# Kernel optimization log

Measured on AMD Instinct MI355X. Metric: run time of the kernel, lower is better.

Reference implementation:

```python
import jax, jax.numpy as jnp
import numpy as np

B, T, C = 1, 2048, 2048
H, KV, D = 16, 4, 128
PAST = 2048


def setup_inputs() -> dict:
    key = jax.random.key(0)
    ks = jax.random.split(key, 11)
    return {
        "x": jax.random.normal(ks[0], (B, T, C), jnp.float32),
        "ve": jax.random.normal(ks[1], (B, T, KV * D), jnp.float32),
        "cos": jax.random.normal(ks[2], (1, T, 1, D // 2), jnp.float32),
        "sin": jax.random.normal(ks[3], (1, T, 1, D // 2), jnp.float32),
        "past_key": jax.random.normal(ks[4], (B, PAST, KV, D), jnp.float32),
        "past_value": jax.random.normal(ks[5], (B, PAST, KV, D), jnp.float32),
        "Wq": jax.random.normal(ks[6], (C, H * D), jnp.float32) * 0.02,
        "Wk": jax.random.normal(ks[7], (C, KV * D), jnp.float32) * 0.02,
        "Wv": jax.random.normal(ks[8], (C, KV * D), jnp.float32) * 0.02,
        "Wo": jax.random.normal(ks[9], (H * D, C), jnp.float32) * 0.02,
        "Wg": jax.random.normal(ks[10], (12, KV), jnp.float32),
    }


def _rmsnorm(x):
    return x * jax.lax.rsqrt(jnp.mean(x * x, axis=-1, keepdims=True) + 1e-6)


def _rope(x, cos, sin):
    # x: (B,T,heads,D); cos/sin: (1,T,1,D//2) broadcast over heads
    d = x.shape[-1] // 2
    x1, x2 = x[..., :d], x[..., d:]
    return jnp.concatenate([x1 * cos + x2 * sin, -x1 * sin + x2 * cos], axis=-1)


def reference(x, ve, cos, sin, past_key, past_value, Wq, Wk, Wv, Wo, Wg):
    Bx, Tx, Cx = x.shape
    G = H // KV
    q = (x @ Wq).reshape(Bx, Tx, H, D)
    k = (x @ Wk).reshape(Bx, Tx, KV, D)
    v = (x @ Wv).reshape(Bx, Tx, KV, D)
    # value-embedding gate: 3*sigmoid over first 12 channels of x
    gate = 3.0 * jax.nn.sigmoid(x[..., :12] @ Wg)  # (B,T,KV)
    v = v + gate[..., None] * ve.reshape(Bx, Tx, KV, D)
    q = _rmsnorm(_rope(q, cos, sin)) * 1.2
    k = _rmsnorm(_rope(k, cos, sin)) * 1.2
    present_key = jnp.concatenate([past_key, k], axis=1)    # (B,S,KV,D)
    present_value = jnp.concatenate([past_value, v], axis=1)
    S = present_key.shape[1]
    q_t = q.transpose(0, 2, 1, 3)                           # (B,H,T,D)
    k_t = present_key.transpose(0, 2, 1, 3)                 # (B,KV,S,D)
    v_t = present_value.transpose(0, 2, 1, 3)
    # GQA expansion: repeat each kv head G times -> (B,H,S,D)
    k_t = jnp.broadcast_to(k_t[:, :, None], (Bx, KV, G, S, D)).reshape(Bx, H, S, D)
    v_t = jnp.broadcast_to(v_t[:, :, None], (Bx, KV, G, S, D)).reshape(Bx, H, S, D)
    scale = D ** -0.5
    scores = jnp.einsum("bhtd,bhsd->bhts", q_t, k_t) * scale
    query_pos = jnp.arange(S - Tx, S)[:, None]
    key_pos = jnp.arange(S)[None, :]
    causal = key_pos <= query_pos                           # (T,S)
    scores = jnp.where(causal[None, None], scores, -jnp.inf)
    w = jax.nn.softmax(scores, axis=-1)
    y = jnp.einsum("bhts,bhsd->bthd", w, v_t).reshape(Bx, Tx, H * D)
    y = y @ Wo
    return (y, present_key, present_value)
```

## Files before the change

kernel.cpp:

```cpp
#include <hip/hip_runtime.h>
#include <hip/hip_bf16.h>
#include <math.h>

typedef __attribute__((ext_vector_type(8))) short short8;
typedef __attribute__((ext_vector_type(4))) short short4v;
typedef __attribute__((ext_vector_type(4))) float f32x4;

#define DEV __device__ __forceinline__

DEV short f2bf(float f) {
  unsigned u = __builtin_bit_cast(unsigned, f);
  unsigned r = (u + 0x7FFFu + ((u >> 16) & 1u)) >> 16;
  return (short)r;
}

DEV short f2h(float f) {
  _Float16 h = (_Float16)f;
  return __builtin_bit_cast(short, h);
}

DEV float h2f(short s) {
  return (float)__builtin_bit_cast(_Float16, s);
}

DEV unsigned cvt_pk_bf16(float lo, float hi) {
  unsigned r;
  asm("v_cvt_pk_bf16_f32 %0, %1, %2" : "=v"(r) : "v"(lo), "v"(hi));
  return r;
}

DEV void gload_lds16(const void* g, void* l) {
  __builtin_amdgcn_global_load_lds((const __attribute__((address_space(1))) void*)g,
                                   (__attribute__((address_space(3))) void*)l, 16, 0, 0);
}

__global__ __launch_bounds__(256) void gemm_bf16(const short* __restrict__ A,
                                                 const short* __restrict__ BT,
                                                 float* __restrict__ C,
                                                 int M, int N, int K) {
  __shared__ __attribute__((aligned(16))) short As[2][128 * 32];
  __shared__ __attribute__((aligned(16))) short Bs[2][128 * 32];
  const int tid = threadIdx.x;
  const int w = tid >> 6, l = tid & 63;
  const int g = l >> 4, lr = l & 15;
  int nbx = gridDim.x, nwg = nbx * gridDim.y;
  int flat = blockIdx.y * nbx + blockIdx.x;
  int qq = nwg >> 3;
  int f2 = (flat & 7) * qq + (flat >> 3);
  const int m0 = (f2 / nbx) * 128, n0 = (f2 % nbx) * 128;
  const int wr = w >> 1, wc = w & 1;
  const int q0 = w * 2, q1 = w * 2 + 1;
  const int e0 = q0 * 512 + l * 8, e1 = q1 * 512 + l * 8;
  const int ra = e0 >> 5, ka = e0 & 31;
  const int rb_ = e1 >> 5, kb_ = e1 & 31;
  f32x4 acc[4][4] = {};

  auto stage = [&](int buf, int k0) {
    gload_lds16(A + (size_t)(m0 + ra) * K + k0 + ka, As[buf] + q0 * 512);
    gload_lds16(BT + (size_t)(n0 + ra) * K + k0 + ka, Bs[buf] + q0 * 512);
    gload_lds16(A + (size_t)(m0 + rb_) * K + k0 + kb_, As[buf] + q1 * 512);
    gload_lds16(BT + (size_t)(n0 + rb_) * K + k0 + kb_, Bs[buf] + q1 * 512);
  };

  stage(0, 0);
  __syncthreads();
  int cur = 0;
  for (int k0 = 0; k0 < K; k0 += 32) {
    if (k0 + 32 < K) stage(cur ^ 1, k0 + 32);
    short8 af[4], bfr[4];
#pragma unroll
    for (int i = 0; i < 4; ++i) {
      af[i] = *(const short8*)(As[cur] + (wr * 64 + i * 16 + lr) * 32 + g * 8);
      bfr[i] = *(const short8*)(Bs[cur] + (wc * 64 + i * 16 + lr) * 32 + g * 8);
    }
#pragma unroll
    for (int mi = 0; mi < 4; ++mi)
#pragma unroll
      for (int ni = 0; ni < 4; ++ni)
        acc[mi][ni] = __builtin_amdgcn_mfma_f32_16x16x32_bf16(af[mi], bfr[ni], acc[mi][ni], 0, 0, 0);
    __syncthreads();
    cur ^= 1;
  }
#pragma unroll
  for (int mi = 0; mi < 4; ++mi)
#pragma unroll
    for (int ni = 0; ni < 4; ++ni) {
      int row = m0 + wr * 64 + mi * 16 + g * 4;
      int col = n0 + wc * 64 + ni * 16 + lr;
#pragma unroll
      for (int r = 0; r < 4; ++r)
        C[(size_t)(row + r) * N + col] = acc[mi][ni][r];
    }
}

__global__ __launch_bounds__(256) void gemm_bf16_k64(const short* __restrict__ A,
                                                     const short* __restrict__ BT,
                                                     float* __restrict__ C,
                                                     int M, int N, int K) {
  __shared__ __attribute__((aligned(16))) short As[2][128 * 64];
  __shared__ __attribute__((aligned(16))) short Bs[2][128 * 64];
  const int tid = threadIdx.x;
  const int w = tid >> 6, l = tid & 63;
  const int g = l >> 4, lr = l & 15;
  int nbx = gridDim.x, nwg = nbx * gridDim.y;
  int flat = blockIdx.y * nbx + blockIdx.x;
  int qq = nwg >> 3;
  int f2 = (flat & 7) * qq + (flat >> 3);
  const int m0 = (f2 / nbx) * 128, n0 = (f2 % nbx) * 128;
  const int wr = w >> 1, wc = w & 1;
  f32x4 acc[4][4] = {};

  auto stage = [&](int buf, int k0) {
#pragma unroll
    for (int it = 0; it < 4; ++it) {
      int idx = it * 256 + tid;
      int row = idx >> 3;
      int colB = (idx & 7) * 16;
      int scol = colB ^ ((row & 7) << 4);
      gload_lds16(A + (size_t)(m0 + row) * K + k0 + (scol >> 1), As[buf] + idx * 8);
      gload_lds16(BT + (size_t)(n0 + row) * K + k0 + (scol >> 1), Bs[buf] + idx * 8);
    }
  };

  stage(0, 0);
  __syncthreads();
  int cur = 0;
  for (int k0 = 0; k0 < K; k0 += 64) {
    if (k0 + 64 < K) stage(cur ^ 1, k0 + 64);
#pragma unroll
    for (int ki = 0; ki < 2; ++ki) {
      short8 af[4], bfr[4];
#pragma unroll
      for (int i = 0; i < 4; ++i) {
        int off = ((wr * 64 + i * 16 + lr) * 128 + ((ki * 64 + g * 16) ^ ((lr & 7) << 4))) >> 1;
        int offb = ((wc * 64 + i * 16 + lr) * 128 + ((ki * 64 + g * 16) ^ ((lr & 7) << 4))) >> 1;
        af[i] = *(const short8*)(As[cur] + off);
        bfr[i] = *(const short8*)(Bs[cur] + offb);
      }
#pragma unroll
      for (int mi = 0; mi < 4; ++mi)
#pragma unroll
        for (int ni = 0; ni < 4; ++ni)
          acc[mi][ni] = __builtin_amdgcn_mfma_f32_16x16x32_bf16(af[mi], bfr[ni], acc[mi][ni], 0, 0, 0);
    }
    __syncthreads();
    cur ^= 1;
  }
#pragma unroll
  for (int mi = 0; mi < 4; ++mi)
#pragma unroll
    for (int ni = 0; ni < 4; ++ni) {
      int row = m0 + wr * 64 + mi * 16 + g * 4;
      int col = n0 + wc * 64 + ni * 16 + lr;
#pragma unroll
      for (int r = 0; r < 4; ++r)
        C[(size_t)(row + r) * N + col] = acc[mi][ni][r];
    }
}

__global__ __launch_bounds__(256) void transpose_all(const float* __restrict__ Wq,
                                                     const float* __restrict__ Wk,
                                                     const float* __restrict__ Wv,
                                                     const float* __restrict__ Wo,
                                                     short* __restrict__ WTqkv,
                                                     short* __restrict__ WToT) {
  __shared__ float tile[32][33];
  int bx = blockIdx.x;
  const float* W;
  short* WT;
  int N, cb;
  if (bx < 64) { W = Wq; WT = WTqkv; N = 2048; cb = bx; }
  else if (bx < 80) { W = Wk; WT = WTqkv + (size_t)2048 * 2048; N = 512; cb = bx - 64; }
  else if (bx < 96) { W = Wv; WT = WTqkv + (size_t)2560 * 2048; N = 512; cb = bx - 80; }
  else { W = Wo; WT = WToT; N = 2048; cb = bx - 96; }
  int tx = threadIdx.x, ty = threadIdx.y;
  int c0 = cb * 32, r0 = blockIdx.y * 32;
#pragma unroll
  for (int i = 0; i < 4; ++i)
    tile[ty + i * 8][tx] = W[(size_t)(r0 + ty + i * 8) * N + c0 + tx];
  __syncthreads();
#pragma unroll
  for (int i = 0; i < 4; ++i)
    WT[(size_t)(c0 + ty + i * 8) * 2048 + r0 + tx] = f2bf(tile[tx][ty + i * 8]);
}

__global__ __launch_bounds__(256) void cvt_x(const float* __restrict__ x,
                                             short* __restrict__ xb, int n4) {
  int i = blockIdx.x * 256 + threadIdx.x;
  if (i >= n4) return;
  float4 v = ((const float4*)x)[i];
  short4v o;
  o.x = f2bf(v.x); o.y = f2bf(v.y); o.z = f2bf(v.z); o.w = f2bf(v.w);
  ((short4v*)xb)[i] = o;
}

__global__ __launch_bounds__(256) void qkv_post(const float* __restrict__ qkv,
                                                const float* __restrict__ cosb,
                                                const float* __restrict__ sinb,
                                                const float* __restrict__ x,
                                                const float* __restrict__ ve,
                                                const float* __restrict__ Wg,
                                                float* __restrict__ outPK,
                                                float* __restrict__ outPV,
                                                short* __restrict__ qb,
                                                short* __restrict__ kb) {
  int gw = (blockIdx.x * 256 + threadIdx.x) >> 6;
  int l = threadIdx.x & 63;
  int t = gw / 24, u = gw - t * 24;
  if (t >= 2048) return;
  if (u < 20) {
    float c = cosb[t * 64 + l], s = sinb[t * 64 + l];
    const float* src = qkv + (size_t)t * 3072 + (u < 16 ? u * 128 : 2048 + (u - 16) * 128);
    float x1 = src[l], x2 = src[64 + l];
    float lo = x1 * c + x2 * s;
    float hi = x2 * c - x1 * s;
    float ss = lo * lo + hi * hi;
#pragma unroll
    for (int d = 1; d < 64; d <<= 1) ss += __shfl_xor(ss, d, 64);
    float r = rsqrtf(ss * (1.0f / 128.0f) + 1e-6f) * 1.2f;
    if (u < 16) {
      const float SCQ = 0.08838834764831845f * 1.4426950408889634f;
      float rq = r * SCQ;
      size_t b = ((size_t)u * 2048 + t) * 128;
      qb[b + l] = f2bf(lo * rq);
      qb[b + 64 + l] = f2bf(hi * rq);
    } else {
      lo *= r; hi *= r;
      int kvh = u - 16;
      size_t b = ((size_t)(2048 + t) * 4 + kvh) * 128;
      outPK[b + l] = lo;
      outPK[b + 64 + l] = hi;
      size_t b2 = ((size_t)kvh * 4096 + 2048 + t) * 128;
      kb[b2 + l] = f2bf(lo);
      kb[b2 + 64 + l] = f2bf(hi);
    }
  } else {
    int kv = u - 20;
    float z = 0.f;
#pragma unroll
    for (int j = 0; j < 12; ++j) z += x[(size_t)t * 2048 + j] * Wg[j * 4 + kv];
    float gate = 3.0f / (1.0f + expf(-z));
    const float* vr = qkv + (size_t)t * 3072 + 2560 + kv * 128;
    const float* vei = ve + (size_t)t * 512 + kv * 128;
    float v0 = vr[l] + gate * vei[l];
    float v1 = vr[64 + l] + gate * vei[64 + l];
    size_t b = ((size_t)(2048 + t) * 4 + kv) * 128;
    outPV[b + l] = v0;
    outPV[b + 64 + l] = v1;
  }
}

__global__ __launch_bounds__(256) void past_copy(const float* __restrict__ pk,
                                                 const float* __restrict__ pv,
                                                 float* __restrict__ outPK,
                                                 float* __restrict__ outPV,
                                                 short* __restrict__ kb) {
  int i = blockIdx.x * 256 + threadIdx.x;
  int d = i & 127, kv = (i >> 7) & 3, s = i >> 9;
  float a = pk[i], b = pv[i];
  outPK[i] = a;
  outPV[i] = b;
  kb[((size_t)kv * 4096 + s) * 128 + d] = f2bf(a);
}

__global__ __launch_bounds__(256) void v_transpose(const float* __restrict__ PV,
                                                   short* __restrict__ vbT) {
  __shared__ float tile[32][33];
  int tx = threadIdx.x, ty = threadIdx.y;
  int c0 = blockIdx.x * 32, r0 = blockIdx.y * 32;
#pragma unroll
  for (int i = 0; i < 4; ++i)
    tile[ty + i * 8][tx] = PV[(size_t)(r0 + ty + i * 8) * 512 + c0 + tx];
  __syncthreads();
#pragma unroll
  for (int i = 0; i < 4; ++i)
    vbT[(size_t)(c0 + ty + i * 8) * 4096 + r0 + tx] = f2bf(tile[tx][ty + i * 8]);
}

__global__ __launch_bounds__(256, 2) void attn(const short* __restrict__ qb,
                                               const short* __restrict__ kb,
                                               const short* __restrict__ vbT,
                                               short* __restrict__ Po,
                                               float* __restrict__ ml) {
  extern __shared__ __attribute__((aligned(16))) short smem[];
  short* Ks = smem;
  short* Vs = smem + 16384;
  const int tid = threadIdx.x, w = tid >> 6, l = tid & 63;
  const int g = l >> 4, lr = l & 15;
  const int lid = blockIdx.x;
  const int qbi = 15 - (lid >> 6);
  const int sub = lid & 63;
  const int h = sub >> 2, cls = sub & 3;
  const int kv = h >> 2;
  const int qw = qbi * 128 + w * 32;
  char* Pw = (char*)(smem + 32768) + w * 2048;
  const short* gK = kb + (size_t)kv * 4096 * 128;
  const short* gV = vbT + (size_t)kv * 128 * 4096;
  const int nT = 34 + 2 * qbi;
  const int cnt = (nT - cls + 3) >> 2;

  short8 aq[2][4];
#pragma unroll
  for (int u = 0; u < 2; ++u)
#pragma unroll
    for (int c4 = 0; c4 < 4; ++c4)
      aq[u][c4] = *(const short8*)(qb + ((size_t)(h * 2048 + qw + u * 16 + lr)) * 128 + c4 * 32 + g * 8);

  float m_r[2] = {-INFINITY, -INFINITY};
  float l_r[2] = {0.f, 0.f};
  f32x4 o[2][8] = {};

  auto stageK = [&](int buf, int s0) {
#pragma unroll
    for (int it = 0; it < 4; ++it) {
      int idx = it * 256 + tid;
      int row = idx >> 4;
      int colB = (idx & 15) * 16;
      int scol = colB ^ ((row & 7) << 4);
      gload_lds16(gK + (size_t)(s0 + row) * 128 + (scol >> 1),
                  Ks + buf * 8192 + (it * 256 + w * 64) * 8);
    }
  };
  auto stageV = [&](int buf, int s0) {
#pragma unroll
    for (int it = 0; it < 4; ++it) {
      int idx = it * 256 + tid;
      int row = idx >> 3;
      int colB = (idx & 7) * 16;
      int scol = colB ^ ((row & 7) << 4);
      gload_lds16(gV + (size_t)row * 4096 + s0 + (scol >> 1),
                  Vs + buf * 8192 + (it * 256 + w * 64) * 8);
    }
  };

  stageK(0, cls * 64);
  stageV(0, cls * 64);
  __syncthreads();
  int cur = 0;
  for (int i = 0; i < cnt; ++i) {
    const int s0 = (cls + 4 * i) * 64;
    if (i + 1 < cnt) {
      stageK(cur ^ 1, s0 + 256);
      stageV(cur ^ 1, s0 + 256);
    }
    f32x4 sc[2][4] = {};
    __builtin_amdgcn_s_setprio(1);
#pragma unroll
    for (int cc = 0; cc < 4; ++cc) {
      const int rb = cur * 8192 + (cc * 16 + lr) * 128;
      short8 bk[4];
#pragma unroll
      for (int c4 = 0; c4 < 4; ++c4)
        bk[c4] = *(const short8*)(Ks + rb + (((c4 * 64 + g * 16) ^ ((lr & 7) << 4)) >> 1));
#pragma unroll
      for (int c4 = 0; c4 < 4; ++c4) {
        sc[0][cc] = __builtin_amdgcn_mfma_f32_16x16x32_bf16(bk[c4], aq[0][c4], sc[0][cc], 0, 0, 0);
        sc[1][cc] = __builtin_amdgcn_mfma_f32_16x16x32_bf16(bk[c4], aq[1][c4], sc[1][cc], 0, 0, 0);
      }
    }
    __builtin_amdgcn_s_setprio(0);
    if (s0 + 63 > 2048 + qw) {
#pragma unroll
      for (int u = 0; u < 2; ++u)
#pragma unroll
        for (int cc = 0; cc < 4; ++cc)
#pragma unroll
          for (int r = 0; r < 4; ++r)
            sc[u][cc][r] = (s0 + cc * 16 + g * 4 + r <= 2048 + qw + u * 16 + lr)
                               ? sc[u][cc][r] : -INFINITY;
    }
    short8 ap[2][2];
#pragma unroll
    for (int u = 0; u < 2; ++u) {
      float pmax = -INFINITY;
#pragma unroll
      for (int cc = 0; cc < 4; ++cc) {
        float a = fmaxf(fmaxf(sc[u][cc][0], sc[u][cc][1]), fmaxf(sc[u][cc][2], sc[u][cc][3]));
        pmax = fmaxf(pmax, a);
      }
      if (!__all(pmax - m_r[u] <= 8.0f)) {
        float tm = fmaxf(pmax, __shfl_xor(pmax, 16, 64));
        tm = fmaxf(tm, __shfl_xor(tm, 32, 64));
        float mn = fmaxf(m_r[u], tm);
        float corr = exp2f(m_r[u] - mn);
        m_r[u] = mn;
        l_r[u] *= corr;
        float co[4];
#pragma unroll
        for (int r = 0; r < 4; ++r) co[r] = __shfl(corr, (l & 48) | (g * 4 + r), 64);
#pragma unroll
        for (int d8 = 0; d8 < 8; ++d8) {
          f32x4 tt = o[u][d8];
#pragma unroll
          for (int r = 0; r < 4; ++r) tt[r] *= co[r];
          o[u][d8] = tt;
        }
      }
      float ps = 0.f;
#pragma unroll
      for (int cc = 0; cc < 4; ++cc) {
        float p0 = exp2f(sc[u][cc][0] - m_r[u]);
        float p1 = exp2f(sc[u][cc][1] - m_r[u]);
        float p2 = exp2f(sc[u][cc][2] - m_r[u]);
        float p3 = exp2f(sc[u][cc][3] - m_r[u]);
        ps += (p0 + p1) + (p2 + p3);
        unsigned pk0 = cvt_pk_bf16(p0, p1);
        unsigned pk1 = cvt_pk_bf16(p2, p3);
        int off8 = (lr * 128 + cc * 32 + g * 8) ^ ((lr & 7) << 4);
        unsigned long long pq = (unsigned long long)pk0 | ((unsigned long long)pk1 << 32);
        *(unsigned long long*)(Pw + off8) = pq;
      }
      l_r[u] += ps;
#pragma unroll
      for (int ks = 0; ks < 2; ++ks)
        ap[u][ks] = *(const short8*)(Pw + ((lr * 128 + ks * 64 + g * 16) ^ ((lr & 7) << 4)));
    }
    __builtin_amdgcn_s_setprio(1);
#pragma unroll
    for (int d8 = 0; d8 < 8; ++d8) {
      const int rb = cur * 8192 + (d8 * 16 + lr) * 64;
      short8 bv0 = *(const short8*)(Vs + rb + (((0 * 64 + g * 16) ^ ((lr & 7) << 4)) >> 1));
      short8 bv1 = *(const short8*)(Vs + rb + (((1 * 64 + g * 16) ^ ((lr & 7) << 4)) >> 1));
      o[0][d8] = __builtin_amdgcn_mfma_f32_16x16x32_bf16(ap[0][0], bv0, o[0][d8], 0, 0, 0);
      o[0][d8] = __builtin_amdgcn_mfma_f32_16x16x32_bf16(ap[0][1], bv1, o[0][d8], 0, 0, 0);
      o[1][d8] = __builtin_amdgcn_mfma_f32_16x16x32_bf16(ap[1][0], bv0, o[1][d8], 0, 0, 0);
      o[1][d8] = __builtin_amdgcn_mfma_f32_16x16x32_bf16(ap[1][1], bv1, o[1][d8], 0, 0, 0);
    }
    __builtin_amdgcn_s_setprio(0);
    __syncthreads();
    cur ^= 1;
  }
#pragma unroll
  for (int u = 0; u < 2; ++u) {
    float ls = l_r[u];
    ls += __shfl_xor(ls, 16, 64);
    ls += __shfl_xor(ls, 32, 64);
    float inv = 1.0f / ls;
    float invo[4];
#pragma unroll
    for (int r = 0; r < 4; ++r) invo[r] = __shfl(inv, (l & 48) | (g * 4 + r), 64);
#pragma unroll
    for (int d8 = 0; d8 < 8; ++d8)
#pragma unroll
      for (int r = 0; r < 4; ++r)
        Po[((size_t)(cls * 16 + h) * 2048 + qw + u * 16 + g * 4 + r) * 128 + d8 * 16 + lr] =
            f2h(o[u][d8][r] * invo[r]);
    if (g == 0) {
      float2 v;
      v.x = m_r[u];
      v.y = ls;
      ((float2*)ml)[(size_t)(cls * 16 + h) * 2048 + qw + u * 16 + lr] = v;
    }
  }
}

__global__ __launch_bounds__(256) void attn_merge(const short* __restrict__ Po,
                                                  const float* __restrict__ ml,
                                                  short* __restrict__ ya) {
  int i = blockIdx.x * 256 + threadIdx.x;
  int q = i >> 8, rem = i & 255, h = rem >> 4, oct = rem & 15;
  float mc[4], lc[4], m = -INFINITY;
#pragma unroll
  for (int c = 0; c < 4; ++c) {
    float2 v = ((const float2*)ml)[(size_t)(c * 16 + h) * 2048 + q];
    mc[c] = v.x; lc[c] = v.y;
    m = fmaxf(m, mc[c]);
  }
  float wsum = 0.f, acc[8] = {};
#pragma unroll
  for (int c = 0; c < 4; ++c) {
    float wc = lc[c] * exp2f(mc[c] - m);
    wsum += wc;
    short8 p = *(const short8*)(Po + ((size_t)(c * 16 + h) * 2048 + q) * 128 + oct * 8);
#pragma unroll
    for (int j = 0; j < 8; ++j) acc[j] += wc * h2f(p[j]);
  }
  float inv = 1.0f / wsum;
  short8 ov;
#pragma unroll
  for (int j = 0; j < 8; ++j) ov[j] = f2bf(acc[j] * inv);
  *(short8*)(ya + (size_t)q * 2048 + h * 128 + oct * 8) = ov;
}

extern "C" void kernel_launch(void* const* d_in, const int* in_sizes, int n_in,
                              void* d_out, int out_size, void* d_ws, size_t ws_size,
                              hipStream_t stream) {
  const float* x = (const float*)d_in[0];
  const float* ve = (const float*)d_in[1];
  const float* cosb = (const float*)d_in[2];
  const float* sinb = (const float*)d_in[3];
  const float* past_key = (const float*)d_in[4];
  const float* past_value = (const float*)d_in[5];
  const float* Wq = (const float*)d_in[6];
  const float* Wk = (const float*)d_in[7];
  const float* Wv = (const float*)d_in[8];
  const float* Wo = (const float*)d_in[9];
  const float* Wg = (const float*)d_in[10];

  float* outY = (float*)d_out;
  float* outPK = outY + 4194304;
  float* outPV = outPK + 2097152;

  short* base = (short*)d_ws;
  short* WToT = base;
  short* WTqkv = base + 4194304;
  short* xb = WTqkv + (size_t)6291456;
  float* qkv = (float*)(xb + (size_t)4194304);
  short* qb = (short*)(qkv + (size_t)6291456);
  short* kb = qb + (size_t)4194304;
  short* vbT = kb + (size_t)2097152;
  short* ya = vbT + (size_t)2097152;
  short* Po = WTqkv;
  float* mlb = (float*)(base + 20971520);

  static bool attr_set = false;
  if (!attr_set) {
    (void)hipFuncSetAttribute((const void*)attn,
                              hipFuncAttributeMaxDynamicSharedMemorySize, 73728);
    attr_set = true;
  }

  cvt_x<<<4096, 256, 0, stream>>>(x, xb, 1048576);
  transpose_all<<<dim3(160, 64), dim3(32, 8), 0, stream>>>(Wq, Wk, Wv, Wo, WTqkv, WToT);

  gemm_bf16<<<dim3(24, 16), 256, 0, stream>>>(xb, WTqkv, qkv, 2048, 3072, 2048);

  qkv_post<<<12288, 256, 0, stream>>>(qkv, cosb, sinb, x, ve, Wg, outPK, outPV, qb, kb);
  past_copy<<<4096, 256, 0, stream>>>(past_key, past_value, outPK, outPV, kb);
  v_transpose<<<dim3(16, 128), dim3(32, 8), 0, stream>>>(outPV, vbT);

  attn<<<1024, 256, 73728, stream>>>(qb, kb, vbT, Po, mlb);
  attn_merge<<<2048, 256, 0, stream>>>(Po, mlb, ya);

  gemm_bf16_k64<<<dim3(16, 16), 256, 0, stream>>>(ya, WToT, outY, 2048, 2048, 2048);
}
```

Measured before the change: 189.5 us.

## Halve attention KV split, fuse x conversion with weight transpose, hoist staging pointers

The attention kernel now splits the key sequence two ways per (head, query block) instead of four, launching 512 blocks. Each block walks twice as many KV tiles and the merge kernel combines two partials instead of four. Separately, the x-to-bf16 conversion and the weight transposes are fused into one prep launch, and the K/V staging address math is precomputed into incrementing pointers. This cuts partial-output traffic, merge work and one launch, but it risks lower parallelism and longer serial chains in attention on a many-CU GPU.

```diff
diff --git a/kernel.cpp b/kernel.cpp
--- a/kernel.cpp
+++ b/kernel.cpp
@@ -158,14 +158,27 @@
     }
 }
 
-__global__ __launch_bounds__(256) void transpose_all(const float* __restrict__ Wq,
-                                                     const float* __restrict__ Wk,
-                                                     const float* __restrict__ Wv,
-                                                     const float* __restrict__ Wo,
-                                                     short* __restrict__ WTqkv,
-                                                     short* __restrict__ WToT) {
+__global__ __launch_bounds__(256) void prep(const float* __restrict__ x,
+                                            short* __restrict__ xb,
+                                            const float* __restrict__ Wq,
+                                            const float* __restrict__ Wk,
+                                            const float* __restrict__ Wv,
+                                            const float* __restrict__ Wo,
+                                            short* __restrict__ WTqkv,
+                                            short* __restrict__ WToT) {
   __shared__ float tile[32][33];
-  int bx = blockIdx.x;
+  int bid = blockIdx.x;
+  int tid = threadIdx.x;
+  if (bid < 4096) {
+    int i = bid * 256 + tid;
+    float4 v = ((const float4*)x)[i];
+    short4v o;
+    o.x = f2bf(v.x); o.y = f2bf(v.y); o.z = f2bf(v.z); o.w = f2bf(v.w);
+    ((short4v*)xb)[i] = o;
+    return;
+  }
+  int b = bid - 4096;
+  int bx = b % 160, by = b / 160;
   const float* W;
   short* WT;
   int N, cb;
@@ -173,8 +186,8 @@
   else if (bx < 80) { W = Wk; WT = WTqkv + (size_t)2048 * 2048; N = 512; cb = bx - 64; }
   else if (bx < 96) { W = Wv; WT = WTqkv + (size_t)2560 * 2048; N = 512; cb = bx - 80; }
   else { W = Wo; WT = WToT; N = 2048; cb = bx - 96; }
-  int tx = threadIdx.x, ty = threadIdx.y;
-  int c0 = cb * 32, r0 = blockIdx.y * 32;
+  int tx = tid & 31, ty = tid >> 5;
+  int c0 = cb * 32, r0 = by * 32;
 #pragma unroll
   for (int i = 0; i < 4; ++i)
     tile[ty + i * 8][tx] = W[(size_t)(r0 + ty + i * 8) * N + c0 + tx];
@@ -182,16 +195,6 @@
 #pragma unroll
   for (int i = 0; i < 4; ++i)
     WT[(size_t)(c0 + ty + i * 8) * 2048 + r0 + tx] = f2bf(tile[tx][ty + i * 8]);
-}
-
-__global__ __launch_bounds__(256) void cvt_x(const float* __restrict__ x,
-                                             short* __restrict__ xb, int n4) {
-  int i = blockIdx.x * 256 + threadIdx.x;
-  if (i >= n4) return;
-  float4 v = ((const float4*)x)[i];
-  short4v o;
-  o.x = f2bf(v.x); o.y = f2bf(v.y); o.z = f2bf(v.z); o.w = f2bf(v.w);
-  ((short4v*)xb)[i] = o;
 }
 
 __global__ __launch_bounds__(256) void qkv_post(const float* __restrict__ qkv,
@@ -266,7 +269,7 @@
 __global__ __launch_bounds__(256) void v_transpose(const float* __restrict__ PV,
                                                    short* __restrict__ vbT) {
   __shared__ float tile[32][33];
-  int tx = threadIdx.x, ty = threadIdx.y;
+  int tx = threadIdx.x & 31, ty = threadIdx.x >> 5;
   int c0 = blockIdx.x * 32, r0 = blockIdx.y * 32;
 #pragma unroll
   for (int i = 0; i < 4; ++i)
@@ -288,16 +291,16 @@
   const int tid = threadIdx.x, w = tid >> 6, l = tid & 63;
   const int g = l >> 4, lr = l & 15;
   const int lid = blockIdx.x;
-  const int qbi = 15 - (lid >> 6);
-  const int sub = lid & 63;
-  const int h = sub >> 2, cls = sub & 3;
+  const int qbi = 15 - (lid >> 5);
+  const int sub = lid & 31;
+  const int h = sub >> 1, cls = sub & 1;
   const int kv = h >> 2;
   const int qw = qbi * 128 + w * 32;
   char* Pw = (char*)(smem + 32768) + w * 2048;
   const short* gK = kb + (size_t)kv * 4096 * 128;
   const short* gV = vbT + (size_t)kv * 128 * 4096;
   const int nT = 34 + 2 * qbi;
-  const int cnt = (nT - cls + 3) >> 2;
+  const int cnt = (nT - cls + 1) >> 1;
 
   short8 aq[2][4];
 #pragma unroll
@@ -310,38 +313,35 @@
   float l_r[2] = {0.f, 0.f};
   f32x4 o[2][8] = {};
 
-  auto stageK = [&](int buf, int s0) {
-#pragma unroll
-    for (int it = 0; it < 4; ++it) {
-      int idx = it * 256 + tid;
-      int row = idx >> 4;
-      int colB = (idx & 15) * 16;
-      int scol = colB ^ ((row & 7) << 4);
-      gload_lds16(gK + (size_t)(s0 + row) * 128 + (scol >> 1),
-                  Ks + buf * 8192 + (it * 256 + w * 64) * 8);
-    }
+  const int rK = tid >> 4, cKs = ((tid & 15) * 16) ^ ((rK & 7) << 4);
+  const int rV = tid >> 3, cVs = ((tid & 7) * 16) ^ ((rV & 7) << 4);
+  const short* kptr = gK + (size_t)(cls * 64 + rK) * 128 + (cKs >> 1);
+  const short* vptr = gV + (size_t)rV * 4096 + cls * 64 + (cVs >> 1);
+  short* kdst = Ks + w * 512;
+  short* vdst = Vs + w * 512;
+
+  auto stageK = [&](int buf) {
+#pragma unroll
+    for (int it = 0; it < 4; ++it)
+      gload_lds16(kptr + it * 2048, kdst + buf * 8192 + it * 2048);
+    kptr += 16384;
   };
-  auto stageV = [&](int buf, int s0) {
-#pragma unroll
-    for (int it = 0; it < 4; ++it) {
-      int idx = it * 256 + tid;
-      int row = idx >> 3;
-      int colB = (idx & 7) * 16;
-      int scol = colB ^ ((row & 7) << 4);
-      gload_lds16(gV + (size_t)row * 4096 + s0 + (scol >> 1),
-                  Vs + buf * 8192 + (it * 256 + w * 64) * 8);
-    }
+  auto stageV = [&](int buf) {
+#pragma unroll
+    for (int it = 0; it < 4; ++it)
+      gload_lds16(vptr + (size_t)it * 131072, vdst + buf * 8192 + it * 2048);
+    vptr += 128;
   };
 
-  stageK(0, cls * 64);
-  stageV(0, cls * 64);
+  stageK(0);
+  stageV(0);
   __syncthreads();
   int cur = 0;
   for (int i = 0; i < cnt; ++i) {
-    const int s0 = (cls + 4 * i) * 64;
+    const int s0 = (cls + 2 * i) * 64;
     if (i + 1 < cnt) {
-      stageK(cur ^ 1, s0 + 256);
-      stageV(cur ^ 1, s0 + 256);
+      stageK(cur ^ 1);
+      stageV(cur ^ 1);
     }
     f32x4 sc[2][4] = {};
     __builtin_amdgcn_s_setprio(1);
@@ -459,16 +459,16 @@
                                                   short* __restrict__ ya) {
   int i = blockIdx.x * 256 + threadIdx.x;
   int q = i >> 8, rem = i & 255, h = rem >> 4, oct = rem & 15;
-  float mc[4], lc[4], m = -INFINITY;
-#pragma unroll
-  for (int c = 0; c < 4; ++c) {
+  float mc[2], lc[2];
+#pragma unroll
+  for (int c = 0; c < 2; ++c) {
     float2 v = ((const float2*)ml)[(size_t)(c * 16 + h) * 2048 + q];
     mc[c] = v.x; lc[c] = v.y;
-    m = fmaxf(m, mc[c]);
-  }
+  }
+  float m = fmaxf(mc[0], mc[1]);
   float wsum = 0.f, acc[8] = {};
 #pragma unroll
-  for (int c = 0; c < 4; ++c) {
+  for (int c = 0; c < 2; ++c) {
     float wc = lc[c] * exp2f(mc[c] - m);
     wsum += wc;
     short8 p = *(const short8*)(Po + ((size_t)(c * 16 + h) * 2048 + q) * 128 + oct * 8);
@@ -520,16 +520,15 @@
     attr_set = true;
   }
 
-  cvt_x<<<4096, 256, 0, stream>>>(x, xb, 1048576);
-  transpose_all<<<dim3(160, 64), dim3(32, 8), 0, stream>>>(Wq, Wk, Wv, Wo, WTqkv, WToT);
+  prep<<<14336, 256, 0, stream>>>(x, xb, Wq, Wk, Wv, Wo, WTqkv, WToT);
 
   gemm_bf16<<<dim3(24, 16), 256, 0, stream>>>(xb, WTqkv, qkv, 2048, 3072, 2048);
 
   qkv_post<<<12288, 256, 0, stream>>>(qkv, cosb, sinb, x, ve, Wg, outPK, outPV, qb, kb);
   past_copy<<<4096, 256, 0, stream>>>(past_key, past_value, outPK, outPV, kb);
-  v_transpose<<<dim3(16, 128), dim3(32, 8), 0, stream>>>(outPV, vbT);
-
-  attn<<<1024, 256, 73728, stream>>>(qb, kb, vbT, Po, mlb);
+  v_transpose<<<dim3(16, 128), 256, 0, stream>>>(outPV, vbT);
+
+  attn<<<512, 256, 73728, stream>>>(qb, kb, vbT, Po, mlb);
   attn_merge<<<2048, 256, 0, stream>>>(Po, mlb, ya);
 
   gemm_bf16_k64<<<dim3(16, 16), 256, 0, stream>>>(ya, WToT, outY, 2048, 2048, 2048);
```

Measured after the change: 185.3 us. 2.2% less time.
